# Performance work log

Hardware: AMD Instinct MI355X
Metric: run time of the kernel (lower is better)

The kernel has to match this reference:

```python
import jax, jax.numpy as jnp
import numpy as np

B = 64          # num_graphs per batch
ADJ = 1000      # adj_shape (nodes per graph)
N = B * ADJ     # total nodes
E = 1 << 20     # edges
M = 32000       # selected (batch, node) pairs
D_IN = 128
D_OUT = 128


def setup_inputs() -> dict:
    key = jax.random.key(0)
    ks = jax.random.split(key, 12)
    inp = {
        "x0": jax.random.normal(ks[0], (N, D_IN), jnp.float32),
        "x1": jax.random.normal(ks[1], (N, D_IN), jnp.float32),
        "edge_index": jax.random.randint(ks[2], (2, E), 0, N, jnp.int64),
        "b_idx0": jax.random.randint(ks[3], (M,), 0, B, jnp.int64),
        "n_idx0": jax.random.randint(ks[4], (M,), 0, ADJ, jnp.int64),
        "b_idx1": jax.random.randint(ks[5], (M,), 0, B, jnp.int64),
        "n_idx1": jax.random.randint(ks[6], (M,), 0, ADJ, jnp.int64),
        "W1": jax.random.normal(ks[7], (D_IN, D_IN), jnp.float32) / np.sqrt(D_IN),
        "b1": jnp.zeros((D_IN,), jnp.float32),
        "W2": jax.random.normal(ks[8], (D_IN, D_IN), jnp.float32) / np.sqrt(D_IN),
        "b2": jnp.zeros((D_IN,), jnp.float32),
        "Wl": jax.random.normal(ks[9], (D_IN, D_OUT), jnp.float32) / np.sqrt(D_IN),
        "bl": jnp.zeros((D_OUT,), jnp.float32),
        "Wfi": jax.random.normal(ks[10], (D_IN, D_OUT), jnp.float32) / np.sqrt(D_IN),
        "bfi": jnp.zeros((D_OUT,), jnp.float32),
    }
    return inp


def _gnn_layer(h, edge_index, W, b):
    # GCN-style message passing: gather source features, scatter-sum to dst,
    # then linear project.  h: [N, d]
    msgs = h[edge_index[0]]                                    # [E, d] gather
    agg = jax.ops.segment_sum(msgs, edge_index[1], num_segments=N)  # [N, d]
    return agg @ W + b


def reference(x0, x1, edge_index, b_idx0, n_idx0, b_idx1, n_idx1,
              W1, b1, W2, b2, Wl, bl, Wfi, bfi):
    # branch i == 0: raw features -> 2D gather -> fc_in
    d0 = x0.reshape(B, ADJ, -1)[b_idx0, n_idx0]                # [M, D_IN]
    d0 = d0 @ Wfi + bfi                                        # [M, D_OUT]

    # branch i == 1 (observ=True): gnn1 -> gnn2 -> 2D gather -> linear
    # (dropout omitted for deterministic reference; p=0.2 at train time)
    h = _gnn_layer(x1, edge_index, W1, b1)
    h = _gnn_layer(h, edge_index, W2, b2)
    d1 = h.reshape(B, ADJ, -1)[b_idx1, n_idx1]                 # [M, D_IN]
    d1 = d1 @ Wl + bl                                          # [M, D_OUT]

    return jnp.stack([d0, d1])                                 # [2, M, D_OUT]
```

## Files before the change

kernel.cpp:

```cpp
#include <hip/hip_runtime.h>
#include <hip/hip_bf16.h>


#define B_    64
#define ADJ_  1000
#define N_    64000
#define E_    (1 << 20)
#define M_    32000
#define DV    128
#define CAP   64
#define CHUNKS 512
#define EPB   (E_ / CHUNKS)
#define FMASK 0x18844221u

typedef __attribute__((ext_vector_type(8))) short short8v;
typedef __attribute__((ext_vector_type(4))) float float4v;

__device__ __forceinline__ float u2f(unsigned int u) {
  union { unsigned int i; float f; } x; x.i = u; return x.f;
}
__device__ __forceinline__ unsigned short f2bf(float f) {
  union { float f; unsigned int i; } x; x.f = f;
  unsigned int r = x.i + 0x7fffu + ((x.i >> 16) & 1u);
  return (unsigned short)(r >> 16);
}
__device__ __forceinline__ unsigned int pack_bf2(float a, float b) {
  __hip_bfloat162 h = __float22bfloat162_rn(float2{a, b});
  union { __hip_bfloat162 h; unsigned int u; } c; c.h = h;
  return c.u;
}

__device__ __forceinline__ int frag_addr(int k, int n) {
  return ((((n >> 4) * 4 + (k >> 5)) * 64 + ((k >> 3) & 3) * 16 + (n & 15)) << 3)
       + (k & 7);
}

__global__ __launch_bounds__(256)
void prep_k(const float* __restrict__ W1, const float* __restrict__ Wfi,
            const float* __restrict__ W2, const float* __restrict__ Wl,
            const float* __restrict__ b2, const float* __restrict__ bl,
            unsigned short* __restrict__ Wbf, float* __restrict__ bc,
            int* __restrict__ counts) {
  int b = blockIdx.x, t = threadIdx.x;
  if (b < 16) {
    const float* W = (b < 8) ? W1 : Wfi;
    unsigned short* out = Wbf + ((b < 8) ? 0 : 16384);
    int base = (b & 7) * 2048 + t * 8;
    float4 f0 = *(const float4*)(W + base);
    float4 f1 = *(const float4*)(W + base + 4);
    float v[8] = {f0.x, f0.y, f0.z, f0.w, f1.x, f1.y, f1.z, f1.w};
#pragma unroll
    for (int u = 0; u < 8; u++) {
      int g = base + u;
      out[frag_addr(g >> 7, g & 127)] = f2bf(v[u]);
    }
  } else if (b < 48) {
    unsigned short* out = Wbf + 2 * 16384;
    int g0 = (b - 16) * 512 + t * 2;
#pragma unroll
    for (int u = 0; u < 2; u++) {
      int g = g0 + u, k = g >> 7, n = g & 127;
      float acc = 0.f;
      for (int j = 0; j < 128; j++) acc += W2[k * 128 + j] * Wl[j * 128 + n];
      out[frag_addr(k, n)] = f2bf(acc);
    }
  } else {
    if (t < 128) {
      float acc = bl[t];
      for (int k = 0; k < 128; k++) acc += b2[k] * Wl[k * 128 + t];
      bc[t] = acc;
    }
  }
  for (int i = b * 256 + t; i < N_; i += 49 * 256) counts[i] = 0;
}

__device__ __forceinline__ void fill_once(const int* __restrict__ ei,
                                          int* __restrict__ counts,
                                          unsigned int* __restrict__ bucket,
                                          int c) {
  const int* srcA = ei;
  const int* dstA = ei + E_;
  int t4 = c * EPB + (int)threadIdx.x * 4;
  int4 d0 = *(const int4*)(dstA + t4);
  int4 s0 = *(const int4*)(srcA + t4);
  int4 d1 = *(const int4*)(dstA + t4 + 1024);
  int4 s1 = *(const int4*)(srcA + t4 + 1024);
#define PROC(D, S) do {                                                         \
    int pos = atomicAdd(&counts[(D)], 1);                                       \
    if (pos < CAP)                                                              \
      __hip_atomic_store(&bucket[(size_t)(D) * CAP + pos], (unsigned int)(S),   \
                         __ATOMIC_RELAXED, __HIP_MEMORY_SCOPE_AGENT);           \
  } while (0)
  PROC(d0.x, s0.x); PROC(d0.y, s0.y); PROC(d0.z, s0.z); PROC(d0.w, s0.w);
  PROC(d1.x, s1.x); PROC(d1.y, s1.y); PROC(d1.z, s1.z); PROC(d1.w, s1.w);
#undef PROC
}

template<bool GATHER, bool ABF16, bool OUTBF16, bool HASBIAS>
__device__ __forceinline__ void gemm_tile(const void* __restrict__ in,
                                          const unsigned short* __restrict__ Wbf,
                                          const float* __restrict__ bias,
                                          void* __restrict__ out_, int tile,
                                          const int* __restrict__ bidx,
                                          const int* __restrict__ nidx,
                                          unsigned short* __restrict__ Bs) {
  int tid  = threadIdx.x;
  int lane = tid & 63;
  int wv   = tid >> 6;
  int m    = lane & 15;
  int q    = lane >> 4;
  int rbase = tile * 64 + wv * 16;
  int r     = rbase + m;

  const short8v* Wv  = (const short8v*)Wbf;
  short8v*       Bsv = (short8v*)Bs;

  short8v w[4];
#pragma unroll
  for (int i = 0; i < 4; i++) w[i] = Wv[tid + i * 256];

  size_t ir;
  if (GATHER) ir = (size_t)bidx[r] * ADJ_ + nidx[r];
  else        ir = (size_t)r;

  short8v af[4];
  if (ABF16) {
    const unsigned short* arow = (const unsigned short*)in + ir * DV;
#pragma unroll
    for (int kc = 0; kc < 4; kc++)
      af[kc] = *(const short8v*)(arow + kc * 32 + q * 8);
  } else {
    const float* arow = (const float*)in + ir * DV;
#pragma unroll
    for (int kc = 0; kc < 4; kc++) {
      const float4* p = (const float4*)(arow + kc * 32 + q * 8);
      float4 f0 = p[0], f1 = p[1];
      union { short8v s; unsigned int u[4]; } t;
      t.u[0] = pack_bf2(f0.x, f0.y);
      t.u[1] = pack_bf2(f0.z, f0.w);
      t.u[2] = pack_bf2(f1.x, f1.y);
      t.u[3] = pack_bf2(f1.z, f1.w);
      af[kc] = t.s;
    }
  }

#pragma unroll
  for (int i = 0; i < 4; i++) Bsv[tid + i * 256] = w[i];
  __syncthreads();

  float4v acc[8];
#pragma unroll
  for (int nb = 0; nb < 8; nb++) acc[nb] = (float4v){0.f, 0.f, 0.f, 0.f};

#pragma unroll
  for (int i = 0; i < 4; i++) w[i] = Wv[1024 + tid + i * 256];

#pragma unroll
  for (int nb = 0; nb < 4; nb++)
#pragma unroll
    for (int kc = 0; kc < 4; kc++) {
      short8v bf = Bsv[(nb * 4 + kc) * 64 + lane];
      acc[nb] = __builtin_amdgcn_mfma_f32_16x16x32_bf16(af[kc], bf, acc[nb], 0, 0, 0);
    }
  __syncthreads();
#pragma unroll
  for (int i = 0; i < 4; i++) Bsv[tid + i * 256] = w[i];
  __syncthreads();
#pragma unroll
  for (int nb = 4; nb < 8; nb++)
#pragma unroll
    for (int kc = 0; kc < 4; kc++) {
      short8v bf = Bsv[((nb - 4) * 4 + kc) * 64 + lane];
      acc[nb] = __builtin_amdgcn_mfma_f32_16x16x32_bf16(af[kc], bf, acc[nb], 0, 0, 0);
    }

#pragma unroll
  for (int nb = 0; nb < 8; nb++) {
    float bvn = HASBIAS ? bias[nb * 16 + m] : 0.f;
    int col = nb * 16 + m;
#pragma unroll
    for (int i = 0; i < 4; i++) {
      int row = rbase + q * 4 + i;
      float v = acc[nb][i] + bvn;
      if (OUTBF16) ((unsigned short*)out_)[(size_t)row * DV + col] = f2bf(v);
      else         ((float*)out_)[(size_t)row * DV + col] = v;
    }
  }
}

__global__ __launch_bounds__(256)
void k1_fused(const int* __restrict__ ei, int* __restrict__ counts,
              unsigned int* __restrict__ bucket,
              const float* __restrict__ x1, const unsigned short* __restrict__ Wbf,
              unsigned int* __restrict__ t_bf,
              const float* __restrict__ x0, const float* __restrict__ bfi,
              float* __restrict__ out0,
              const int* __restrict__ b0, const int* __restrict__ n0i) {
  __shared__ unsigned short Bs[8192];
  unsigned int rem = blockIdx.x & 31, hi = blockIdx.x >> 5;
  int below = __popc(FMASK & ((1u << rem) - 1u));
  if ((FMASK >> rem) & 1u) { fill_once(ei, counts, bucket, hi * 8 + below); return; }
  int o = hi * 24 + (int)(rem - below);
  if (o < 1000)
    gemm_tile<false, false, true, false>(x1, Wbf, nullptr, t_bf, o, nullptr, nullptr, Bs);
  else if (o < 1500)
    gemm_tile<true, false, false, true>(x0, Wbf + 16384, bfi, out0, o - 1000, b0, n0i, Bs);
}

template<bool GATHER, bool ABF16, bool OUTBF16, bool HASBIAS>
__global__ __launch_bounds__(256)
void gemm_k(const void* __restrict__ in, const unsigned short* __restrict__ Wbf,
            const float* __restrict__ bias, void* __restrict__ out_,
            const int* __restrict__ bidx, const int* __restrict__ nidx) {
  __shared__ unsigned short Bs[8192];
  gemm_tile<GATHER, ABF16, OUTBF16, HASBIAS>(in, Wbf, bias, out_, blockIdx.x, bidx, nidx, Bs);
}

template<bool OUTBF16, bool SEL>
__global__ __launch_bounds__(256)
void aggregate_k(const unsigned int* __restrict__ x,
                 const int* __restrict__ counts,
                 const unsigned int* __restrict__ bucket,
                 const float* __restrict__ bias, void* __restrict__ out_,
                 const int* __restrict__ bidx, const int* __restrict__ nidx) {
  int w    = (blockIdx.x * 256 + threadIdx.x) >> 6;
  int lane = threadIdx.x & 63;
  int node = SEL ? (bidx[w] * ADJ_ + nidx[w]) : w;
  int cnt = counts[node]; cnt = min(cnt, CAP);
  int mysrc = (int)bucket[(size_t)node * CAP + lane];

  float2 acc;
  if (bias) { float2 bv = ((const float2*)bias)[lane]; acc.x = bv.x; acc.y = bv.y; }
  else      { acc.x = 0.f; acc.y = 0.f; }

#define BATCH16(BASE) do {                                               \
    unsigned int uu[16];                                                 \
    _Pragma("unroll")                                                    \
    for (int i = 0; i < 16; i++) {                                       \
      int s = __shfl(mysrc, (BASE) + i, 64) & 0xffff;                    \
      uu[i] = x[(size_t)s * 64 + lane];                                  \
    }                                                                    \
    _Pragma("unroll")                                                    \
    for (int i = 0; i < 16; i++) {                                       \
      unsigned int mm = ((BASE) + i < cnt) ? uu[i] : 0u;                 \
      acc.x += u2f(mm << 16);                                            \
      acc.y += u2f(mm & 0xffff0000u);                                    \
    }                                                                    \
  } while (0)

  BATCH16(0);
  if (cnt > 16) BATCH16(16);
  if (cnt > 32) BATCH16(32);
  if (cnt > 48) BATCH16(48);
#undef BATCH16

  if (OUTBF16) ((unsigned int*)out_)[(size_t)w * 64 + lane] = pack_bf2(acc.x, acc.y);
  else         ((float2*)out_)[(size_t)w * 64 + lane] = acc;
}

extern "C" void kernel_launch(void* const* d_in, const int* in_sizes, int n_in,
                              void* d_out, int out_size, void* d_ws, size_t ws_size,
                              hipStream_t stream) {
  const float* x0  = (const float*)d_in[0];
  const float* x1  = (const float*)d_in[1];
  const int*   ei  = (const int*)  d_in[2];
  const int*   b0  = (const int*)  d_in[3];
  const int*   n0i = (const int*)  d_in[4];
  const int*   b1  = (const int*)  d_in[5];
  const int*   n1i = (const int*)  d_in[6];
  const float* W1  = (const float*)d_in[7];
  const float* bb1 = (const float*)d_in[8];
  const float* W2  = (const float*)d_in[9];
  const float* bb2 = (const float*)d_in[10];
  const float* Wl  = (const float*)d_in[11];
  const float* bl  = (const float*)d_in[12];
  const float* Wfi = (const float*)d_in[13];
  const float* bfi = (const float*)d_in[14];
  float* out = (float*)d_out;

  unsigned int*   t_bf   = (unsigned int*)d_ws;
  unsigned int*   sel_bf = t_bf;
  unsigned int*   h_bf   = t_bf + (size_t)N_ * 64;
  int*            counts = (int*)(h_bf + (size_t)N_ * 64);
  unsigned int*   bucket = (unsigned int*)(counts + N_);
  unsigned short* Wbf    = (unsigned short*)(bucket + (size_t)N_ * CAP);
  float*          bc     = (float*)(Wbf + 3 * 16384);

  prep_k<<<49, 256, 0, stream>>>(W1, Wfi, W2, Wl, bb2, bl, Wbf, bc, counts);

  k1_fused<<<2048, 256, 0, stream>>>(ei, counts, bucket, x1, Wbf, t_bf,
                                     x0, bfi, out, b0, n0i);

  aggregate_k<true, false><<<N_ / 4, 256, 0, stream>>>(t_bf, counts, bucket,
                                                       bb1, h_bf, nullptr, nullptr);
  aggregate_k<true, true><<<M_ / 4, 256, 0, stream>>>(h_bf, counts, bucket,
                                                      nullptr, sel_bf, b1, n1i);
  gemm_k<false, true, false, true><<<M_ / 64, 256, 0, stream>>>(sel_bf, Wbf + 2 * 16384,
                                                                bc, out + (size_t)M_ * DV,
                                                                nullptr, nullptr);
}
```

Baseline: 268.0 us.

## Use 16-bit edge buckets, finer fill chunks, and count-guarded aggregation loads

Edge buckets now store 16-bit source ids instead of 32-bit, which halves bucket write and read traffic; node ids below 64000 fit in 16 bits. The fill phase moves from 512 chunks to 4096 chunks with one edge per thread, interleaved as 8 fill blocks per 3 GEMM tiles, to spread the atomics more evenly across the GEMM work. Aggregation now loads only neighbors below the node's count, using a 32-wide unrolled batch plus a tail loop, instead of always loading in batches of 16 and masking. The W2*Wl precompute in prep_k is vectorized over 4 columns per thread. The costs are more blocks and less memory-level parallelism per fill thread, plus more divergent control flow in aggregation.

```diff
diff --git a/kernel.cpp b/kernel.cpp
--- a/kernel.cpp
+++ b/kernel.cpp
@@ -9,9 +9,8 @@
 #define M_    32000
 #define DV    128
 #define CAP   64
-#define CHUNKS 512
+#define CHUNKS 4096
 #define EPB   (E_ / CHUNKS)
-#define FMASK 0x18844221u
 
 typedef __attribute__((ext_vector_type(8))) short short8v;
 typedef __attribute__((ext_vector_type(4))) float float4v;
@@ -54,16 +53,21 @@
       int g = base + u;
       out[frag_addr(g >> 7, g & 127)] = f2bf(v[u]);
     }
-  } else if (b < 48) {
+  } else if (b < 32) {
     unsigned short* out = Wbf + 2 * 16384;
-    int g0 = (b - 16) * 512 + t * 2;
-#pragma unroll
-    for (int u = 0; u < 2; u++) {
-      int g = g0 + u, k = g >> 7, n = g & 127;
-      float acc = 0.f;
-      for (int j = 0; j < 128; j++) acc += W2[k * 128 + j] * Wl[j * 128 + n];
-      out[frag_addr(k, n)] = f2bf(acc);
-    }
+    int g0 = (b - 16) * 1024 + t * 4;
+    int k = g0 >> 7, n = g0 & 127;
+    float4 acc = {0.f, 0.f, 0.f, 0.f};
+    for (int j = 0; j < 128; j++) {
+      float w2 = W2[k * 128 + j];
+      float4 wl = *(const float4*)(Wl + j * 128 + n);
+      acc.x += w2 * wl.x; acc.y += w2 * wl.y;
+      acc.z += w2 * wl.z; acc.w += w2 * wl.w;
+    }
+    out[frag_addr(k, n + 0)] = f2bf(acc.x);
+    out[frag_addr(k, n + 1)] = f2bf(acc.y);
+    out[frag_addr(k, n + 2)] = f2bf(acc.z);
+    out[frag_addr(k, n + 3)] = f2bf(acc.w);
   } else {
     if (t < 128) {
       float acc = bl[t];
@@ -71,29 +75,20 @@
       bc[t] = acc;
     }
   }
-  for (int i = b * 256 + t; i < N_; i += 49 * 256) counts[i] = 0;
+  for (int i = b * 256 + t; i < N_; i += 33 * 256) counts[i] = 0;
 }
 
 __device__ __forceinline__ void fill_once(const int* __restrict__ ei,
                                           int* __restrict__ counts,
-                                          unsigned int* __restrict__ bucket,
+                                          unsigned short* __restrict__ bucket,
                                           int c) {
-  const int* srcA = ei;
-  const int* dstA = ei + E_;
-  int t4 = c * EPB + (int)threadIdx.x * 4;
-  int4 d0 = *(const int4*)(dstA + t4);
-  int4 s0 = *(const int4*)(srcA + t4);
-  int4 d1 = *(const int4*)(dstA + t4 + 1024);
-  int4 s1 = *(const int4*)(srcA + t4 + 1024);
-#define PROC(D, S) do {                                                         \
-    int pos = atomicAdd(&counts[(D)], 1);                                       \
-    if (pos < CAP)                                                              \
-      __hip_atomic_store(&bucket[(size_t)(D) * CAP + pos], (unsigned int)(S),   \
-                         __ATOMIC_RELAXED, __HIP_MEMORY_SCOPE_AGENT);           \
-  } while (0)
-  PROC(d0.x, s0.x); PROC(d0.y, s0.y); PROC(d0.z, s0.z); PROC(d0.w, s0.w);
-  PROC(d1.x, s1.x); PROC(d1.y, s1.y); PROC(d1.z, s1.z); PROC(d1.w, s1.w);
-#undef PROC
+  int e = c * EPB + (int)threadIdx.x;
+  int d = ei[E_ + e];
+  int s = ei[e];
+  int pos = atomicAdd(&counts[d], 1);
+  if (pos < CAP)
+    __hip_atomic_store(&bucket[(size_t)d * CAP + pos], (unsigned short)s,
+                       __ATOMIC_RELAXED, __HIP_MEMORY_SCOPE_AGENT);
 }
 
 template<bool GATHER, bool ABF16, bool OUTBF16, bool HASBIAS>
@@ -190,17 +185,16 @@
 
 __global__ __launch_bounds__(256)
 void k1_fused(const int* __restrict__ ei, int* __restrict__ counts,
-              unsigned int* __restrict__ bucket,
+              unsigned short* __restrict__ bucket,
               const float* __restrict__ x1, const unsigned short* __restrict__ Wbf,
               unsigned int* __restrict__ t_bf,
               const float* __restrict__ x0, const float* __restrict__ bfi,
               float* __restrict__ out0,
               const int* __restrict__ b0, const int* __restrict__ n0i) {
   __shared__ unsigned short Bs[8192];
-  unsigned int rem = blockIdx.x & 31, hi = blockIdx.x >> 5;
-  int below = __popc(FMASK & ((1u << rem) - 1u));
-  if ((FMASK >> rem) & 1u) { fill_once(ei, counts, bucket, hi * 8 + below); return; }
-  int o = hi * 24 + (int)(rem - below);
+  int g = blockIdx.x / 11, rem = blockIdx.x % 11;
+  if (rem < 8) { fill_once(ei, counts, bucket, g * 8 + rem); return; }
+  int o = g * 3 + rem - 8;
   if (o < 1000)
     gemm_tile<false, false, true, false>(x1, Wbf, nullptr, t_bf, o, nullptr, nullptr, Bs);
   else if (o < 1500)
@@ -220,7 +214,7 @@
 __global__ __launch_bounds__(256)
 void aggregate_k(const unsigned int* __restrict__ x,
                  const int* __restrict__ counts,
-                 const unsigned int* __restrict__ bucket,
+                 const unsigned short* __restrict__ bucket,
                  const float* __restrict__ bias, void* __restrict__ out_,
                  const int* __restrict__ bidx, const int* __restrict__ nidx) {
   int w    = (blockIdx.x * 256 + threadIdx.x) >> 6;
@@ -233,26 +227,25 @@
   if (bias) { float2 bv = ((const float2*)bias)[lane]; acc.x = bv.x; acc.y = bv.y; }
   else      { acc.x = 0.f; acc.y = 0.f; }
 
-#define BATCH16(BASE) do {                                               \
-    unsigned int uu[16];                                                 \
-    _Pragma("unroll")                                                    \
-    for (int i = 0; i < 16; i++) {                                       \
-      int s = __shfl(mysrc, (BASE) + i, 64) & 0xffff;                    \
-      uu[i] = x[(size_t)s * 64 + lane];                                  \
-    }                                                                    \
-    _Pragma("unroll")                                                    \
-    for (int i = 0; i < 16; i++) {                                       \
-      unsigned int mm = ((BASE) + i < cnt) ? uu[i] : 0u;                 \
-      acc.x += u2f(mm << 16);                                            \
-      acc.y += u2f(mm & 0xffff0000u);                                    \
-    }                                                                    \
-  } while (0)
-
-  BATCH16(0);
-  if (cnt > 16) BATCH16(16);
-  if (cnt > 32) BATCH16(32);
-  if (cnt > 48) BATCH16(48);
-#undef BATCH16
+  unsigned int uu[32];
+#pragma unroll
+  for (int i = 0; i < 32; i++)
+    if (i < cnt) {
+      int s = __shfl(mysrc, i, 64);
+      uu[i] = x[(size_t)s * 64 + lane];
+    }
+#pragma unroll
+  for (int i = 0; i < 32; i++)
+    if (i < cnt) {
+      acc.x += u2f(uu[i] << 16);
+      acc.y += u2f(uu[i] & 0xffff0000u);
+    }
+  for (int d = 32; d < cnt; d++) {
+    int s = __shfl(mysrc, d, 64);
+    unsigned int u = x[(size_t)s * 64 + lane];
+    acc.x += u2f(u << 16);
+    acc.y += u2f(u & 0xffff0000u);
+  }
 
   if (OUTBF16) ((unsigned int*)out_)[(size_t)w * 64 + lane] = pack_bf2(acc.x, acc.y);
   else         ((float2*)out_)[(size_t)w * 64 + lane] = acc;
@@ -282,13 +275,13 @@
   unsigned int*   sel_bf = t_bf;
   unsigned int*   h_bf   = t_bf + (size_t)N_ * 64;
   int*            counts = (int*)(h_bf + (size_t)N_ * 64);
-  unsigned int*   bucket = (unsigned int*)(counts + N_);
-  unsigned short* Wbf    = (unsigned short*)(bucket + (size_t)N_ * CAP);
+  unsigned short* bucket = (unsigned short*)(counts + N_);
+  unsigned short* Wbf    = bucket + (size_t)N_ * CAP;
   float*          bc     = (float*)(Wbf + 3 * 16384);
 
-  prep_k<<<49, 256, 0, stream>>>(W1, Wfi, W2, Wl, bb2, bl, Wbf, bc, counts);
-
-  k1_fused<<<2048, 256, 0, stream>>>(ei, counts, bucket, x1, Wbf, t_bf,
+  prep_k<<<33, 256, 0, stream>>>(W1, Wfi, W2, Wl, bb2, bl, Wbf, bc, counts);
+
+  k1_fused<<<5632, 256, 0, stream>>>(ei, counts, bucket, x1, Wbf, t_bf,
                                      x0, bfi, out, b0, n0i);
 
   aggregate_k<true, false><<<N_ / 4, 256, 0, stream>>>(t_bf, counts, bucket,
```

Measured after the change: 258.5 us. -3.5%, faster.
